# Kernel tuning notes

Hardware: AMD Instinct MI355X
Metric: run time of the kernel (lower is better)

## Reference

```python
import jax, jax.numpy as jnp
import numpy as np

N = 500000   # nodes per graph batch
E = 8000000  # edges per graph batch
B = 4096     # number of graphs
C = 2        # node feature dim
D = 2        # edge feature dim


def setup_inputs() -> dict:
    key = jax.random.key(0)
    ks = jax.random.split(key, 16)
    inp = {
        "x_a": jax.random.normal(ks[0], (N, C), jnp.float32),
        "edge_index_a": jax.random.randint(ks[1], (2, E), 0, N, jnp.int32),
        "edge_attr_a": jax.random.normal(ks[2], (E, D), jnp.float32),
        "batch_a": jnp.sort(jax.random.randint(ks[3], (N,), 0, B, jnp.int32)),
        "x_b": jax.random.normal(ks[4], (N, C), jnp.float32),
        "edge_index_b": jax.random.randint(ks[5], (2, E), 0, N, jnp.int32),
        "edge_attr_b": jax.random.normal(ks[6], (E, D), jnp.float32),
        "batch_b": jnp.sort(jax.random.randint(ks[7], (N,), 0, B, jnp.int32)),
        "targets": jax.random.normal(ks[8], (B,), jnp.float32),
        "num_graphs": B,
        # CGConv params: lin_f, lin_s each Linear(2*C+D=6 -> C)
        "Wf": jax.random.normal(ks[9], (2 * C + D, C), jnp.float32) * 0.4,
        "bf": jnp.zeros((C,), jnp.float32),
        "Ws": jax.random.normal(ks[10], (2 * C + D, C), jnp.float32) * 0.4,
        "bs": jnp.zeros((C,), jnp.float32),
        # l1: Linear(2 -> 3), l2: Linear(6 -> 1)
        "W1": jax.random.normal(ks[11], (C, 3), jnp.float32) * 0.5,
        "b1": jnp.zeros((3,), jnp.float32),
        "W2": jax.random.normal(ks[12], (6, 1), jnp.float32) * 0.4,
        "b2": jnp.zeros((1,), jnp.float32),
    }
    return inp


def cg_conv(x, edge_index, edge_attr, Wf, bf, Ws, bs):
    # PyG CGConv: out_i = x_i + sum_{j->i} sigmoid(lin_f(z)) * softplus(lin_s(z)),
    # z = [x_i, x_j, e_ij]; source_to_target flow => i = edge_index[1].
    src, dst = edge_index[0], edge_index[1]
    z = jnp.concatenate([x[dst], x[src], edge_attr], axis=1)  # [E, 6]
    m = jax.nn.sigmoid(z @ Wf + bf) * jax.nn.softplus(z @ Ws + bs)  # [E, C]
    agg = jax.ops.segment_sum(m, dst, num_segments=x.shape[0])
    return x + agg


def branch(x, edge_index, edge_attr, batch, num_graphs,
           Wf, bf, Ws, bs, W1, b1):
    h = cg_conv(x, edge_index, edge_attr, Wf, bf, Ws, bs)
    h = jax.nn.relu(h @ W1 + b1)  # [N, 3]
    sums = jax.ops.segment_sum(h, batch, num_segments=num_graphs)
    cnts = jax.ops.segment_sum(jnp.ones((h.shape[0],), h.dtype), batch,
                               num_segments=num_graphs)
    return sums / jnp.maximum(cnts, 1.0)[:, None]  # global_mean_pool [B, 3]


def reference(x_a, edge_index_a, edge_attr_a, batch_a,
              x_b, edge_index_b, edge_attr_b, batch_b,
              targets, num_graphs,
              Wf, bf, Ws, bs, W1, b1, W2, b2):
    out_1 = branch(x_a, edge_index_a, edge_attr_a, batch_a, num_graphs,
                   Wf, bf, Ws, bs, W1, b1)
    out_2 = branch(x_b, edge_index_b, edge_attr_b, batch_b, num_graphs,
                   Wf, bf, Ws, bs, W1, b1)
    out = jnp.concatenate([out_1, out_2], axis=1)  # [B, 6]
    out = jax.nn.relu(out @ W2 + b2)               # [B, 1]
    loss = jnp.mean((out[:, 0] - targets) ** 2)
    return out, loss
```

## Files before the change

### kernel.cpp

```cpp
#include <hip/hip_runtime.h>

#define N_NODES 500000
#define N_EDGES 8000000
#define N_GRAPHS 4096

#define NB 128
#define BIN_SHIFT 12
#define BIN_NODES 4096
#define NBINS 123
#define BIN_CAP 66560
#define T_EDGES 4096
#define P1_THREADS 512
#define EPT (T_EDGES / P1_THREADS)
#define P1_GRID ((N_EDGES + T_EDGES - 1) / T_EDGES)
#define K 4
#define P2_GRID (NBINS * K)
#define SLICE_F (BIN_NODES * 2)
#define FXS 131072.0f
#define FXI (1.0f / 131072.0f)
#define M_MAX 250.0f
#define OVF_CAP 8192
#define SGRID ((N_NODES + 255) / 256)

#define OFF_CURS_A   0
#define OFF_CURS_B   512
#define OFF_OVFC_A   1024
#define OFF_OVFC_B   1280
#define ZERO_SMALL   1536
#define OFF_STARTS_A 4096
#define OFF_STARTS_B 20736
#define OFF_MEAN_A   37376
#define OFF_MEAN_B   86528
#define OFF_OVF_A    135680
#define OFF_OVF_B    266752
#define OFF_SCRATCH  397824
#define OFF_BINS     16519680
#define WS_NEED      82014720ull

__device__ __forceinline__ float2 ntload_f2(const float2* p) {
    unsigned long long v = __builtin_nontemporal_load((const unsigned long long*)p);
    float2 r;
    r.x = __uint_as_float((unsigned int)v);
    r.y = __uint_as_float((unsigned int)(v >> 32));
    return r;
}

__global__ __launch_bounds__(512, 8) void p1_kernel(
    const float* __restrict__ x, const int* __restrict__ ei,
    const float* __restrict__ ea,
    const float* __restrict__ Wf, const float* __restrict__ bfv,
    const float* __restrict__ Ws, const float* __restrict__ bsv,
    unsigned long long* __restrict__ bins, unsigned int* __restrict__ cursors,
    unsigned int* __restrict__ ovf_cnt, float4* __restrict__ ovf)
{
    __shared__ unsigned long long sorted[T_EDGES];
    __shared__ unsigned int whist[8][NB];
    __shared__ unsigned int base[NB];
    __shared__ unsigned int cur[NB];
    __shared__ unsigned int gbase[NB];
    __shared__ unsigned int ntot_s;
    unsigned char* binof = (unsigned char*)whist;

    int t = threadIdx.x;
    int wave = t >> 6;
    int ebase = blockIdx.x * T_EDGES;

    for (int i = t; i < 8 * NB; i += P1_THREADS) ((unsigned int*)whist)[i] = 0;
    __syncthreads();

    int d[EPT];
#pragma unroll
    for (int i = 0; i < EPT; ++i) {
        int e = ebase + i * P1_THREADS + t;
        d[i] = (e < N_EDGES) ? __builtin_nontemporal_load(ei + N_EDGES + e) : -1;
        if (d[i] >= 0)
            atomicAdd(&whist[wave][((unsigned)d[i]) >> BIN_SHIFT], 1u);
    }
    __syncthreads();

    unsigned g0 = 0, g1 = 0;
    if (t < 64) {
        unsigned tot0 = 0, tot1 = 0;
#pragma unroll
        for (int w = 0; w < 8; ++w) { tot0 += whist[w][2*t]; tot1 += whist[w][2*t+1]; }
        unsigned pair = tot0 + tot1;
        unsigned v = pair;
#pragma unroll
        for (int off = 1; off < 64; off <<= 1) {
            unsigned u = __shfl_up(v, off);
            if (t >= off) v += u;
        }
        unsigned excl = v - pair;
        base[2*t]   = excl;        cur[2*t]   = excl;
        base[2*t+1] = excl + tot0; cur[2*t+1] = excl + tot0;
        if (t == 63) ntot_s = v;
        g0 = tot0 ? atomicAdd(&cursors[2*t],   tot0) : 0u;
        g1 = tot1 ? atomicAdd(&cursors[2*t+1], tot1) : 0u;
    }
    __syncthreads();

    float wf[12], wsv[12];
#pragma unroll
    for (int i = 0; i < 12; ++i) { wf[i] = Wf[i]; wsv[i] = Ws[i]; }
    float bf0 = bfv[0], bf1 = bfv[1], bs0 = bsv[0], bs1 = bsv[1];

#pragma unroll
    for (int i = 0; i < EPT; ++i) {
        int e = ebase + i * P1_THREADS + t;
        if (e >= N_EDGES) continue;
        int dst = d[i];
        int src = __builtin_nontemporal_load(ei + e);
        float2 xd = ((const float2*)x)[dst];
        float2 xs = ((const float2*)x)[src];
        float2 ev = ntload_f2((const float2*)ea + e);
        float z0 = xd.x, z1 = xd.y, z2 = xs.x, z3 = xs.y, z4 = ev.x, z5 = ev.y;

        float f0 = bf0 + z0*wf[0] + z1*wf[2] + z2*wf[4] + z3*wf[6] + z4*wf[8]  + z5*wf[10];
        float f1 = bf1 + z0*wf[1] + z1*wf[3] + z2*wf[5] + z3*wf[7] + z4*wf[9]  + z5*wf[11];
        float s0 = bs0 + z0*wsv[0] + z1*wsv[2] + z2*wsv[4] + z3*wsv[6] + z4*wsv[8]  + z5*wsv[10];
        float s1 = bs1 + z0*wsv[1] + z1*wsv[3] + z2*wsv[5] + z3*wsv[7] + z4*wsv[9]  + z5*wsv[11];

        float m0 = (1.f/(1.f+__expf(-f0))) * (fmaxf(s0,0.f) + __logf(1.f+__expf(-fabsf(s0))));
        float m1 = (1.f/(1.f+__expf(-f1))) * (fmaxf(s1,0.f) + __logf(1.f+__expf(-fabsf(s1))));

        int b = (int)((unsigned)dst >> BIN_SHIFT);
        unsigned slot = atomicAdd(&cur[b], 1u);
        unsigned long long pk = 0ull;
        if (m0 < M_MAX && m1 < M_MAX) {
            unsigned fx0 = __float2uint_rn(m0 * FXS);
            unsigned fx1 = __float2uint_rn(m1 * FXS);
            pk = (unsigned long long)((unsigned)dst & (BIN_NODES - 1))
               | ((unsigned long long)fx0 << 12)
               | ((unsigned long long)fx1 << 37);
        } else {
            unsigned oi = atomicAdd(ovf_cnt, 1u);
            if (oi < OVF_CAP) ovf[oi] = make_float4(__int_as_float(dst), m0, m1, 0.f);
        }
        sorted[slot] = pk;
        binof[slot] = (unsigned char)b;
    }
    if (t < 64) { gbase[2*t] = g0; gbase[2*t+1] = g1; }
    __syncthreads();

    int ntot = (int)ntot_s;
    for (int p = t; p < ntot; p += P1_THREADS) {
        int lo = (int)binof[p];
        unsigned gpos = gbase[lo] + (unsigned)(p - (int)base[lo]);
        unsigned long long v = sorted[p];
        if (gpos < BIN_CAP) {
            __builtin_nontemporal_store(v, &bins[(size_t)lo * BIN_CAP + gpos]);
        } else {
            int local = (int)(v & (BIN_NODES - 1));
            float m0 = (float)((unsigned)((v >> 12) & 0x1FFFFFFu)) * FXI;
            float m1 = (float)((unsigned)((v >> 37) & 0x1FFFFFFu)) * FXI;
            int dst = (lo << BIN_SHIFT) + local;
            unsigned oi = atomicAdd(ovf_cnt, 1u);
            if (oi < OVF_CAP) ovf[oi] = make_float4(__int_as_float(dst), m0, m1, 0.f);
        }
    }
}

__global__ __launch_bounds__(512, 8) void p2_kernel(
    const unsigned long long* __restrict__ bins,
    const unsigned int* __restrict__ cursors,
    float* __restrict__ scratch)
{
    __shared__ float acc[SLICE_F];
    int b = blockIdx.x >> 2;
    int k = blockIdx.x & 3;
    int t = threadIdx.x;
#pragma unroll
    for (int i = t; i < SLICE_F; i += 512) acc[i] = 0.f;
    __syncthreads();

    int n = (int)min(cursors[b], (unsigned)BIN_CAP);
    int s = (n * k) / K, e = (n * (k + 1)) / K;
    const unsigned long long* bp = bins + (size_t)b * BIN_CAP;
    for (int i = s + t; i < e; i += 512) {
        unsigned long long v = __builtin_nontemporal_load(bp + i);
        int local = (int)(v & (BIN_NODES - 1));
        float m0 = (float)((unsigned)((v >> 12) & 0x1FFFFFFu)) * FXI;
        float m1 = (float)((unsigned)((v >> 37) & 0x1FFFFFFu)) * FXI;
        atomicAdd(&acc[local],             m0);
        atomicAdd(&acc[BIN_NODES + local], m1);
    }
    __syncthreads();

    float4* dst = (float4*)(scratch + (size_t)(b * K + k) * SLICE_F);
    const float4* src = (const float4*)acc;
#pragma unroll
    for (int i = t; i < SLICE_F / 4; i += 512) dst[i] = src[i];
}

__global__ __launch_bounds__(256) void ovf_kernel(
    const float4* __restrict__ ovf, const unsigned int* __restrict__ ovf_cnt,
    float* __restrict__ scratch)
{
    int n = (int)min(*ovf_cnt, (unsigned)OVF_CAP);
    for (int i = threadIdx.x; i < n; i += 256) {
        float4 r = ovf[i];
        int dst = __float_as_int(r.x);
        int b = dst >> BIN_SHIFT, local = dst & (BIN_NODES - 1);
        float* p = scratch + (size_t)(b * K) * SLICE_F;
        unsafeAtomicAdd(p + local,             r.y);
        unsafeAtomicAdd(p + BIN_NODES + local, r.z);
    }
}

__global__ __launch_bounds__(256) void starts_kernel(
    const int* __restrict__ ba, const int* __restrict__ bb,
    unsigned int* __restrict__ sa, unsigned int* __restrict__ sb)
{
    int blk = blockIdx.x;
    const int* batch = ba;
    unsigned int* starts = sa;
    if (blk >= SGRID) { blk -= SGRID; batch = bb; starts = sb; }
    int i = blk * 256 + threadIdx.x;
    if (i >= N_NODES) return;
    int b1 = batch[i];
    if (i == 0) {
        for (int g = 0; g <= b1; ++g) starts[g] = 0;
    } else {
        int b0 = batch[i - 1];
        for (int g = b0 + 1; g <= b1; ++g) starts[g] = i;
    }
    if (i == N_NODES - 1) {
        for (int g = b1 + 1; g <= N_GRAPHS; ++g) starts[g] = N_NODES;
    }
}

__global__ __launch_bounds__(256) void pool2_kernel(
    const float* __restrict__ x, const float* __restrict__ scratch,
    const unsigned int* __restrict__ starts,
    const float* __restrict__ W1, const float* __restrict__ b1,
    float* __restrict__ mean_out)
{
    int wave = threadIdx.x >> 6, lane = threadIdx.x & 63;
    int g = blockIdx.x * 4 + wave;

    float w00 = W1[0], w01 = W1[1], w02 = W1[2];
    float w10 = W1[3], w11 = W1[4], w12 = W1[5];
    float c0 = b1[0], c1 = b1[1], c2 = b1[2];

    int s = (int)starts[g], e = (int)starts[g + 1];
    float a0 = 0.f, a1 = 0.f, a2 = 0.f;
    for (int i = s + lane; i < e; i += 64) {
        int b = i >> BIN_SHIFT, local = i & (BIN_NODES - 1);
        const float* sl = scratch + (size_t)(b * K) * SLICE_F + local;
        float h0 = sl[0] + sl[SLICE_F] + sl[2*SLICE_F] + sl[3*SLICE_F];
        float h1 = sl[BIN_NODES] + sl[BIN_NODES + SLICE_F]
                 + sl[BIN_NODES + 2*SLICE_F] + sl[BIN_NODES + 3*SLICE_F];
        float2 xv = ((const float2*)x)[i];
        h0 += xv.x;
        h1 += xv.y;
        a0 += fmaxf(h0*w00 + h1*w10 + c0, 0.f);
        a1 += fmaxf(h0*w01 + h1*w11 + c1, 0.f);
        a2 += fmaxf(h0*w02 + h1*w12 + c2, 0.f);
    }
#pragma unroll
    for (int off = 32; off; off >>= 1) {
        a0 += __shfl_down(a0, off);
        a1 += __shfl_down(a1, off);
        a2 += __shfl_down(a2, off);
    }
    if (lane == 0) {
        float inv = 1.0f / fmaxf((float)(e - s), 1.0f);
        mean_out[3*(size_t)g]     = a0 * inv;
        mean_out[3*(size_t)g + 1] = a1 * inv;
        mean_out[3*(size_t)g + 2] = a2 * inv;
    }
}

__global__ __launch_bounds__(1024) void final_kernel(
    const float* __restrict__ ma, const float* __restrict__ mb,
    const float* __restrict__ W2, const float* __restrict__ b2,
    const float* __restrict__ targets,
    float* __restrict__ out)
{
    __shared__ float red[1024];
    float w0 = W2[0], w1 = W2[1], w2 = W2[2], w3 = W2[3], w4 = W2[4], w5 = W2[5];
    float bias = b2[0];

    float lsum = 0.f;
    for (int g = threadIdx.x; g < N_GRAPHS; g += 1024) {
        float v = bias
                + ma[3*(size_t)g]*w0 + ma[3*(size_t)g+1]*w1 + ma[3*(size_t)g+2]*w2
                + mb[3*(size_t)g]*w3 + mb[3*(size_t)g+1]*w4 + mb[3*(size_t)g+2]*w5;
        v = fmaxf(v, 0.f);
        out[g] = v;
        float d = v - targets[g];
        lsum += d * d;
    }
    red[threadIdx.x] = lsum;
    __syncthreads();
#pragma unroll
    for (int off = 512; off; off >>= 1) {
        if (threadIdx.x < (unsigned)off) red[threadIdx.x] += red[threadIdx.x + off];
        __syncthreads();
    }
    if (threadIdx.x == 0) out[N_GRAPHS] = red[0] * (1.0f / (float)N_GRAPHS);
}

#define FB_SCALE 4194304.0f
#define FB_INV   2.384185791015625e-07f

__global__ __launch_bounds__(256) void fb_edge_kernel(
    const float* __restrict__ x, const int* __restrict__ ei,
    const float* __restrict__ ea,
    const float* __restrict__ Wf, const float* __restrict__ bfv,
    const float* __restrict__ Ws, const float* __restrict__ bsv,
    unsigned long long* __restrict__ agg)
{
    float wf[12], ws[12];
#pragma unroll
    for (int i = 0; i < 12; ++i) { wf[i] = Wf[i]; ws[i] = Ws[i]; }
    float bf0 = bfv[0], bf1 = bfv[1], bs0 = bsv[0], bs1 = bsv[1];

    int e = blockIdx.x * 256 + threadIdx.x;
    int src = ei[e];
    int dst = ei[N_EDGES + e];
    float2 xd = ((const float2*)x)[dst];
    float2 xs = ((const float2*)x)[src];
    float2 ev = ((const float2*)ea)[e];
    float z0 = xd.x, z1 = xd.y, z2 = xs.x, z3 = xs.y, z4 = ev.x, z5 = ev.y;

    float f0 = bf0 + z0*wf[0] + z1*wf[2] + z2*wf[4] + z3*wf[6] + z4*wf[8]  + z5*wf[10];
    float f1 = bf1 + z0*wf[1] + z1*wf[3] + z2*wf[5] + z3*wf[7] + z4*wf[9]  + z5*wf[11];
    float s0 = bs0 + z0*ws[0] + z1*ws[2] + z2*ws[4] + z3*ws[6] + z4*ws[8]  + z5*ws[10];
    float s1 = bs1 + z0*ws[1] + z1*ws[3] + z2*ws[5] + z3*ws[7] + z4*ws[9]  + z5*ws[11];

    float m0 = (1.f/(1.f+__expf(-f0))) * (fmaxf(s0,0.f) + __logf(1.f+__expf(-fabsf(s0))));
    float m1 = (1.f/(1.f+__expf(-f1))) * (fmaxf(s1,0.f) + __logf(1.f+__expf(-fabsf(s1))));

    unsigned int fx0 = __float2uint_rn(m0 * FB_SCALE);
    unsigned int fx1 = __float2uint_rn(m1 * FB_SCALE);
    atomicAdd(&agg[dst], (unsigned long long)fx0 | ((unsigned long long)fx1 << 32));
}

__global__ __launch_bounds__(64) void fb_pool_kernel(
    const float* __restrict__ x, const unsigned long long* __restrict__ agg,
    const int* __restrict__ batch,
    const float* __restrict__ W1, const float* __restrict__ b1,
    float* __restrict__ mean_out)
{
    int b = blockIdx.x;
    float w00 = W1[0], w01 = W1[1], w02 = W1[2];
    float w10 = W1[3], w11 = W1[4], w12 = W1[5];
    float c0 = b1[0], c1 = b1[1], c2 = b1[2];

    int lo = 0, hi = N_NODES;
    while (lo < hi) { int mid = (lo + hi) >> 1; if (batch[mid] < b) lo = mid + 1; else hi = mid; }
    int seg_s = lo;
    hi = N_NODES;
    while (lo < hi) { int mid = (lo + hi) >> 1; if (batch[mid] < b + 1) lo = mid + 1; else hi = mid; }
    int seg_e = lo;

    float a0 = 0.f, a1 = 0.f, a2 = 0.f;
    for (int i = seg_s + (int)threadIdx.x; i < seg_e; i += 64) {
        unsigned long long v = agg[i];
        float g0 = (float)(unsigned int)(v & 0xffffffffull) * FB_INV;
        float g1 = (float)(unsigned int)(v >> 32) * FB_INV;
        float2 xv = ((const float2*)x)[i];
        float h0 = xv.x + g0, h1 = xv.y + g1;
        a0 += fmaxf(h0*w00 + h1*w10 + c0, 0.f);
        a1 += fmaxf(h0*w01 + h1*w11 + c1, 0.f);
        a2 += fmaxf(h0*w02 + h1*w12 + c2, 0.f);
    }
#pragma unroll
    for (int off = 32; off; off >>= 1) {
        a0 += __shfl_down(a0, off);
        a1 += __shfl_down(a1, off);
        a2 += __shfl_down(a2, off);
    }
    if (threadIdx.x == 0) {
        float inv = 1.0f / fmaxf((float)(seg_e - seg_s), 1.0f);
        mean_out[3*(size_t)b]     = a0 * inv;
        mean_out[3*(size_t)b + 1] = a1 * inv;
        mean_out[3*(size_t)b + 2] = a2 * inv;
    }
}

extern "C" void kernel_launch(void* const* d_in, const int* in_sizes, int n_in,
                              void* d_out, int out_size, void* d_ws, size_t ws_size,
                              hipStream_t stream) {
    const float* x_a     = (const float*)d_in[0];
    const int*   ei_a    = (const int*)  d_in[1];
    const float* ea_a    = (const float*)d_in[2];
    const int*   batch_a = (const int*)  d_in[3];
    const float* x_b     = (const float*)d_in[4];
    const int*   ei_b    = (const int*)  d_in[5];
    const float* ea_b    = (const float*)d_in[6];
    const int*   batch_b = (const int*)  d_in[7];
    const float* targets = (const float*)d_in[8];
    const float* Wf = (const float*)d_in[10];
    const float* bf = (const float*)d_in[11];
    const float* Ws = (const float*)d_in[12];
    const float* bs = (const float*)d_in[13];
    const float* W1 = (const float*)d_in[14];
    const float* b1 = (const float*)d_in[15];
    const float* W2 = (const float*)d_in[16];
    const float* b2 = (const float*)d_in[17];
    float* out = (float*)d_out;
    char* ws = (char*)d_ws;

    if (ws_size >= WS_NEED) {
        unsigned int* curs_a   = (unsigned int*)(ws + OFF_CURS_A);
        unsigned int* curs_b   = (unsigned int*)(ws + OFF_CURS_B);
        unsigned int* ovfc_a   = (unsigned int*)(ws + OFF_OVFC_A);
        unsigned int* ovfc_b   = (unsigned int*)(ws + OFF_OVFC_B);
        unsigned int* starts_a = (unsigned int*)(ws + OFF_STARTS_A);
        unsigned int* starts_b = (unsigned int*)(ws + OFF_STARTS_B);
        float* mean_a = (float*)(ws + OFF_MEAN_A);
        float* mean_b = (float*)(ws + OFF_MEAN_B);
        float4* ovf_a = (float4*)(ws + OFF_OVF_A);
        float4* ovf_b = (float4*)(ws + OFF_OVF_B);
        float* scratch = (float*)(ws + OFF_SCRATCH);
        unsigned long long* bins = (unsigned long long*)(ws + OFF_BINS);

        hipMemsetAsync(ws, 0, ZERO_SMALL, stream);

        starts_kernel<<<2 * SGRID, 256, 0, stream>>>(batch_a, batch_b, starts_a, starts_b);

        p1_kernel<<<P1_GRID, P1_THREADS, 0, stream>>>(x_a, ei_a, ea_a, Wf, bf, Ws, bs,
                                                      bins, curs_a, ovfc_a, ovf_a);
        p2_kernel<<<P2_GRID, 512, 0, stream>>>(bins, curs_a, scratch);
        ovf_kernel<<<1, 256, 0, stream>>>(ovf_a, ovfc_a, scratch);
        pool2_kernel<<<N_GRAPHS / 4, 256, 0, stream>>>(x_a, scratch, starts_a, W1, b1, mean_a);

        p1_kernel<<<P1_GRID, P1_THREADS, 0, stream>>>(x_b, ei_b, ea_b, Wf, bf, Ws, bs,
                                                      bins, curs_b, ovfc_b, ovf_b);
        p2_kernel<<<P2_GRID, 512, 0, stream>>>(bins, curs_b, scratch);
        ovf_kernel<<<1, 256, 0, stream>>>(ovf_b, ovfc_b, scratch);
        pool2_kernel<<<N_GRAPHS / 4, 256, 0, stream>>>(x_b, scratch, starts_b, W1, b1, mean_b);

        final_kernel<<<1, 1024, 0, stream>>>(mean_a, mean_b, W2, b2, targets, out);
    } else {
        unsigned long long* aggu_a = (unsigned long long*)ws;
        unsigned long long* aggu_b = aggu_a + (size_t)N_NODES;
        float* mean_a = (float*)(aggu_b + (size_t)N_NODES);
        float* mean_b = mean_a + 3 * (size_t)N_GRAPHS;

        hipMemsetAsync(ws, 0, 2 * (size_t)N_NODES * sizeof(unsigned long long), stream);
        fb_edge_kernel<<<N_EDGES / 256, 256, 0, stream>>>(x_a, ei_a, ea_a, Wf, bf, Ws, bs, aggu_a);
        fb_edge_kernel<<<N_EDGES / 256, 256, 0, stream>>>(x_b, ei_b, ea_b, Wf, bf, Ws, bs, aggu_b);
        fb_pool_kernel<<<N_GRAPHS, 64, 0, stream>>>(x_a, aggu_a, batch_a, W1, b1, mean_a);
        fb_pool_kernel<<<N_GRAPHS, 64, 0, stream>>>(x_b, aggu_b, batch_b, W1, b1, mean_b);
        final_kernel<<<1, 1024, 0, stream>>>(mean_a, mean_b, W2, b2, targets, out);
    }
}
```

Baseline: 717.7 us.

## Batch edge gathers ahead of compute and interleave scratch slices as float2

Halves edges per block in the binning kernel, loads src indices with dst, and issues all x[dst], x[src] and edge-attr gathers for a thread's edges before the compute loop to raise memory-level parallelism. The per-bin scratch slices are written interleaved (h0,h1 pairs), so the pooling kernel reads one float2 per slice instead of two scalar loads, and the overflow kernel adds into the new layout. The cost is more registers per thread and twice as many blocks doing global cursor atomics.

```diff
diff --git a/kernel.cpp b/kernel.cpp
--- a/kernel.cpp
+++ b/kernel.cpp
@@ -9,7 +9,7 @@
 #define BIN_NODES 4096
 #define NBINS 123
 #define BIN_CAP 66560
-#define T_EDGES 4096
+#define T_EDGES 2048
 #define P1_THREADS 512
 #define EPT (T_EDGES / P1_THREADS)
 #define P1_GRID ((N_EDGES + T_EDGES - 1) / T_EDGES)
@@ -68,11 +68,14 @@
     for (int i = t; i < 8 * NB; i += P1_THREADS) ((unsigned int*)whist)[i] = 0;
     __syncthreads();
 
-    int d[EPT];
+    int d[EPT], s[EPT];
 #pragma unroll
     for (int i = 0; i < EPT; ++i) {
         int e = ebase + i * P1_THREADS + t;
-        d[i] = (e < N_EDGES) ? __builtin_nontemporal_load(ei + N_EDGES + e) : -1;
+        if (e < N_EDGES) {
+            d[i] = __builtin_nontemporal_load(ei + N_EDGES + e);
+            s[i] = __builtin_nontemporal_load(ei + e);
+        } else { d[i] = -1; s[i] = 0; }
         if (d[i] >= 0)
             atomicAdd(&whist[wave][((unsigned)d[i]) >> BIN_SHIFT], 1u);
     }
@@ -99,6 +102,17 @@
     }
     __syncthreads();
 
+    float2 xdv[EPT], xsv[EPT], eav[EPT];
+#pragma unroll
+    for (int i = 0; i < EPT; ++i) {
+        int e = ebase + i * P1_THREADS + t;
+        if (e < N_EDGES) {
+            xdv[i] = ((const float2*)x)[d[i]];
+            xsv[i] = ((const float2*)x)[s[i]];
+            eav[i] = ntload_f2((const float2*)ea + e);
+        }
+    }
+
     float wf[12], wsv[12];
 #pragma unroll
     for (int i = 0; i < 12; ++i) { wf[i] = Wf[i]; wsv[i] = Ws[i]; }
@@ -109,11 +123,9 @@
         int e = ebase + i * P1_THREADS + t;
         if (e >= N_EDGES) continue;
         int dst = d[i];
-        int src = __builtin_nontemporal_load(ei + e);
-        float2 xd = ((const float2*)x)[dst];
-        float2 xs = ((const float2*)x)[src];
-        float2 ev = ntload_f2((const float2*)ea + e);
-        float z0 = xd.x, z1 = xd.y, z2 = xs.x, z3 = xs.y, z4 = ev.x, z5 = ev.y;
+        float z0 = xdv[i].x, z1 = xdv[i].y;
+        float z2 = xsv[i].x, z3 = xsv[i].y;
+        float z4 = eav[i].x, z5 = eav[i].y;
 
         float f0 = bf0 + z0*wf[0] + z1*wf[2] + z2*wf[4] + z3*wf[6] + z4*wf[8]  + z5*wf[10];
         float f1 = bf1 + z0*wf[1] + z1*wf[3] + z2*wf[5] + z3*wf[7] + z4*wf[9]  + z5*wf[11];
@@ -187,9 +199,12 @@
     __syncthreads();
 
     float4* dst = (float4*)(scratch + (size_t)(b * K + k) * SLICE_F);
-    const float4* src = (const float4*)acc;
-#pragma unroll
-    for (int i = t; i < SLICE_F / 4; i += 512) dst[i] = src[i];
+#pragma unroll
+    for (int i = t; i < BIN_NODES / 2; i += 512) {
+        float a0 = acc[2*i],             a1 = acc[2*i + 1];
+        float b0 = acc[BIN_NODES + 2*i], b1 = acc[BIN_NODES + 2*i + 1];
+        dst[i] = make_float4(a0, b0, a1, b1);
+    }
 }
 
 __global__ __launch_bounds__(256) void ovf_kernel(
@@ -201,9 +216,9 @@
         float4 r = ovf[i];
         int dst = __float_as_int(r.x);
         int b = dst >> BIN_SHIFT, local = dst & (BIN_NODES - 1);
-        float* p = scratch + (size_t)(b * K) * SLICE_F;
-        unsafeAtomicAdd(p + local,             r.y);
-        unsafeAtomicAdd(p + BIN_NODES + local, r.z);
+        float* p = scratch + (size_t)(b * K) * SLICE_F + 2 * local;
+        unsafeAtomicAdd(p,     r.y);
+        unsafeAtomicAdd(p + 1, r.z);
     }
 }
 
@@ -242,17 +257,19 @@
     float w10 = W1[3], w11 = W1[4], w12 = W1[5];
     float c0 = b1[0], c1 = b1[1], c2 = b1[2];
 
+    const float2* sc2 = (const float2*)scratch;
     int s = (int)starts[g], e = (int)starts[g + 1];
     float a0 = 0.f, a1 = 0.f, a2 = 0.f;
     for (int i = s + lane; i < e; i += 64) {
         int b = i >> BIN_SHIFT, local = i & (BIN_NODES - 1);
-        const float* sl = scratch + (size_t)(b * K) * SLICE_F + local;
-        float h0 = sl[0] + sl[SLICE_F] + sl[2*SLICE_F] + sl[3*SLICE_F];
-        float h1 = sl[BIN_NODES] + sl[BIN_NODES + SLICE_F]
-                 + sl[BIN_NODES + 2*SLICE_F] + sl[BIN_NODES + 3*SLICE_F];
+        size_t f2base = (size_t)(b * K) * BIN_NODES + local;
+        float2 g0 = sc2[f2base];
+        float2 g1 = sc2[f2base + BIN_NODES];
+        float2 g2 = sc2[f2base + 2 * BIN_NODES];
+        float2 g3 = sc2[f2base + 3 * BIN_NODES];
         float2 xv = ((const float2*)x)[i];
-        h0 += xv.x;
-        h1 += xv.y;
+        float h0 = xv.x + g0.x + g1.x + g2.x + g3.x;
+        float h1 = xv.y + g0.y + g1.y + g2.y + g3.y;
         a0 += fmaxf(h0*w00 + h1*w10 + c0, 0.f);
         a1 += fmaxf(h0*w01 + h1*w11 + c1, 0.f);
         a2 += fmaxf(h0*w02 + h1*w12 + c2, 0.f);
```

Result: slower. 775.9 us (+8.1%).
